# Kernel tuning notes

Hardware: AMD Instinct MI355X
Metric: run time of the kernel (lower is better)

Reference implementation:

```python
import jax, jax.numpy as jnp
import numpy as np

D_MODEL = 1024
NUM_HEADS = 16
D_K = D_MODEL // NUM_HEADS
D_FF = 4096
THETA = 10000.0
EPS = 1e-5


def rmsnorm(x, w):
    ms = jnp.mean(jnp.square(x), axis=-1, keepdims=True)
    return x * jax.lax.rsqrt(ms + EPS) * w


def rope(x, pos):
    # x: [B, H, S, d_k]; pos: [S]
    half = x.shape[-1] // 2
    inv_freq = THETA ** (-jnp.arange(half, dtype=x.dtype) * 2.0 / x.shape[-1])  # [half]
    ang = pos.astype(x.dtype)[:, None] * inv_freq[None, :]  # [S, half]
    cos, sin = jnp.cos(ang), jnp.sin(ang)
    xe, xo = x[..., 0::2], x[..., 1::2]
    oe = xe * cos - xo * sin
    oo = xe * sin + xo * cos
    return jnp.stack([oe, oo], axis=-1).reshape(x.shape)


def setup_inputs() -> dict:
    key = jax.random.key(0)
    ks = jax.random.split(key, 10)
    std_d = 1.0 / np.sqrt(D_MODEL)
    std_f = 1.0 / np.sqrt(D_FF)
    B, S = 4, 2048
    return {
        "x": jax.random.normal(ks[0], (B, S, D_MODEL), dtype=jnp.float32),
        "token_positions": jnp.arange(S, dtype=jnp.int32),
        "q_proj": jax.random.normal(ks[1], (D_MODEL, D_MODEL), dtype=jnp.float32) * std_d,
        "k_proj": jax.random.normal(ks[2], (D_MODEL, D_MODEL), dtype=jnp.float32) * std_d,
        "v_proj": jax.random.normal(ks[3], (D_MODEL, D_MODEL), dtype=jnp.float32) * std_d,
        "o_proj": jax.random.normal(ks[4], (D_MODEL, D_MODEL), dtype=jnp.float32) * std_d,
        "w1": jax.random.normal(ks[5], (D_FF, D_MODEL), dtype=jnp.float32) * std_d,
        "w2": jax.random.normal(ks[6], (D_MODEL, D_FF), dtype=jnp.float32) * std_f,
        "w3": jax.random.normal(ks[7], (D_FF, D_MODEL), dtype=jnp.float32) * std_d,
        "ln1_w": jnp.ones((D_MODEL,), dtype=jnp.float32),
        "ln2_w": jnp.ones((D_MODEL,), dtype=jnp.float32),
    }


def reference(x, token_positions, q_proj, k_proj, v_proj, o_proj, w1, w2, w3, ln1_w, ln2_w):
    B, S, _ = x.shape
    x_ln = rmsnorm(x, ln1_w)
    q = x_ln @ q_proj.T
    k = x_ln @ k_proj.T
    v = x_ln @ v_proj.T
    # [B, S, D] -> [B, H, S, d_k]
    def split_heads(t):
        return t.reshape(B, S, NUM_HEADS, D_K).transpose(0, 2, 1, 3)
    q, k, v = split_heads(q), split_heads(k), split_heads(v)
    q = rope(q, token_positions)
    k = rope(k, token_positions)
    scores = jnp.einsum("bhqd,bhkd->bhqk", q, k) / jnp.sqrt(jnp.asarray(D_K, x.dtype))
    causal = jnp.tril(jnp.ones((S, S), dtype=bool))
    scores = jnp.where(causal, scores, -jnp.inf)
    attn = jax.nn.softmax(scores, axis=-1)
    out = jnp.einsum("bhqk,bhkd->bhqd", attn, v)
    out = out.transpose(0, 2, 1, 3).reshape(B, S, D_MODEL)
    x = x + out @ o_proj.T
    x_ln2 = rmsnorm(x, ln2_w)
    u = x_ln2 @ w1.T
    vff = x_ln2 @ w3.T
    ff = (u * jax.nn.sigmoid(u)) * vff
    return x + ff @ w2.T
```

## Files before the change

kernel.cpp:

```cpp
#include <hip/hip_runtime.h>
#include <hip/hip_bf16.h>


typedef unsigned short u16;
typedef __attribute__((ext_vector_type(8))) short short8;
typedef __attribute__((ext_vector_type(4))) float f32x4;
typedef __attribute__((ext_vector_type(16))) float f32x16;

#define MFMA16(a, b, c) __builtin_amdgcn_mfma_f32_16x16x32_bf16(a, b, c, 0, 0, 0)
#define MFMA32(a, b, c) __builtin_amdgcn_mfma_f32_32x32x16_bf16(a, b, c, 0, 0, 0)

__device__ __forceinline__ u16 f2b(float f) {
  union { float f; unsigned u; } x; x.f = f;
  unsigned r = x.u + 0x7FFFu + ((x.u >> 16) & 1u);
  return (u16)(r >> 16);
}
__device__ __forceinline__ float b2f(u16 h) {
  union { unsigned u; float f; } x; x.u = ((unsigned)h) << 16;
  return x.f;
}
__device__ __forceinline__ unsigned pkbf(float a, float b) {
  __hip_bfloat162 h = __float22bfloat162_rn(make_float2(a, b));
  union { __hip_bfloat162 h; unsigned u; } cv; cv.h = h;
  return cv.u;
}
__device__ __forceinline__ void async16(const void* g, void* l) {
  __builtin_amdgcn_global_load_lds(
      (const __attribute__((address_space(1))) void*)g,
      (__attribute__((address_space(3))) void*)l, 16, 0, 0);
}

template <int MODE>
__global__ __launch_bounds__(256, 2) void gemm_bt(
    const u16* __restrict__ A, const u16* __restrict__ B,
    u16* __restrict__ Cb, float* __restrict__ Cf, const float* __restrict__ R,
    int M, int N, int K) {
  __shared__ __align__(16) u16 As[128 * 64];
  __shared__ __align__(16) u16 Bs[128 * 64];
  const int tid = threadIdx.x;
  const int l = tid & 63, w = tid >> 6;
  const int wr = w & 1, wc = w >> 1;
  const int lr = l & 31, lh = l >> 5;
  const size_t m0 = (size_t)blockIdx.y * 128, n0 = (size_t)blockIdx.x * 128;
  f32x16 acc[2][2] = {};
  for (int k0 = 0; k0 < K; k0 += 64) {
#pragma unroll
    for (int t = 0; t < 4; ++t) {
      int c = t * 256 + tid;
      int r = c >> 3;
      int gc = ((c & 7) ^ (r & 7)) << 3;
      async16(A + (m0 + r) * (size_t)K + k0 + gc, &As[c * 8]);
    }
#pragma unroll
    for (int t = 0; t < 4; ++t) {
      int c = t * 256 + tid;
      int r = c >> 3;
      int gc = ((c & 7) ^ (r & 7)) << 3;
      async16(B + (n0 + r) * (size_t)K + k0 + gc, &Bs[c * 8]);
    }
    __syncthreads();
#pragma unroll
    for (int c = 0; c < 4; ++c) {
      const int c8 = c * 2 + lh;
      short8 af[2], bfr[2];
#pragma unroll
      for (int mi = 0; mi < 2; ++mi) {
        int r = wr * 64 + mi * 32 + lr;
        af[mi] = *(const short8*)&As[r * 64 + ((c8 ^ (r & 7)) << 3)];
      }
#pragma unroll
      for (int ni = 0; ni < 2; ++ni) {
        int r = wc * 64 + ni * 32 + lr;
        bfr[ni] = *(const short8*)&Bs[r * 64 + ((c8 ^ (r & 7)) << 3)];
      }
#pragma unroll
      for (int mi = 0; mi < 2; ++mi)
#pragma unroll
        for (int ni = 0; ni < 2; ++ni)
          acc[mi][ni] = MFMA32(af[mi], bfr[ni], acc[mi][ni]);
    }
    __syncthreads();
  }
#pragma unroll
  for (int mi = 0; mi < 2; ++mi)
#pragma unroll
    for (int ni = 0; ni < 2; ++ni) {
      size_t n = n0 + wc * 64 + ni * 32 + lr;
#pragma unroll
      for (int reg = 0; reg < 16; ++reg) {
        size_t m = m0 + wr * 64 + mi * 32 + (reg & 3) + 8 * (reg >> 2) + 4 * lh;
        float v = acc[mi][ni][reg];
        if (MODE == 0)
          Cb[m * (size_t)N + n] = f2b(v);
        else
          Cf[m * (size_t)N + n] = v + R[m * (size_t)N + n];
      }
    }
}

__global__ __launch_bounds__(256, 2) void ffn_gemm(
    const u16* __restrict__ A, const u16* __restrict__ B1,
    const u16* __restrict__ B3, u16* __restrict__ Hout, int M, int N, int K) {
  __shared__ __align__(16) u16 As[128 * 64];
  __shared__ __align__(16) u16 B1s[128 * 64];
  __shared__ __align__(16) u16 B3s[128 * 64];
  const int tid = threadIdx.x;
  const int l = tid & 63, w = tid >> 6;
  const int wr = w & 1, wc = w >> 1;
  const int lr = l & 31, lh = l >> 5;
  const size_t m0 = (size_t)blockIdx.y * 128, n0 = (size_t)blockIdx.x * 128;
  f32x16 a1[2][2] = {}, a3[2][2] = {};
  for (int k0 = 0; k0 < K; k0 += 64) {
#pragma unroll
    for (int t = 0; t < 4; ++t) {
      int c = t * 256 + tid;
      int r = c >> 3;
      int gc = ((c & 7) ^ (r & 7)) << 3;
      async16(A + (m0 + r) * (size_t)K + k0 + gc, &As[c * 8]);
      async16(B1 + (n0 + r) * (size_t)K + k0 + gc, &B1s[c * 8]);
      async16(B3 + (n0 + r) * (size_t)K + k0 + gc, &B3s[c * 8]);
    }
    __syncthreads();
#pragma unroll
    for (int c = 0; c < 4; ++c) {
      const int c8 = c * 2 + lh;
      short8 af[2], b1f[2], b3f[2];
#pragma unroll
      for (int mi = 0; mi < 2; ++mi) {
        int r = wr * 64 + mi * 32 + lr;
        af[mi] = *(const short8*)&As[r * 64 + ((c8 ^ (r & 7)) << 3)];
      }
#pragma unroll
      for (int ni = 0; ni < 2; ++ni) {
        int r = wc * 64 + ni * 32 + lr;
        b1f[ni] = *(const short8*)&B1s[r * 64 + ((c8 ^ (r & 7)) << 3)];
        b3f[ni] = *(const short8*)&B3s[r * 64 + ((c8 ^ (r & 7)) << 3)];
      }
#pragma unroll
      for (int mi = 0; mi < 2; ++mi)
#pragma unroll
        for (int ni = 0; ni < 2; ++ni) {
          a1[mi][ni] = MFMA32(af[mi], b1f[ni], a1[mi][ni]);
          a3[mi][ni] = MFMA32(af[mi], b3f[ni], a3[mi][ni]);
        }
    }
    __syncthreads();
  }
#pragma unroll
  for (int mi = 0; mi < 2; ++mi)
#pragma unroll
    for (int ni = 0; ni < 2; ++ni) {
      size_t n = n0 + wc * 64 + ni * 32 + lr;
#pragma unroll
      for (int reg = 0; reg < 16; ++reg) {
        size_t m = m0 + wr * 64 + mi * 32 + (reg & 3) + 8 * (reg >> 2) + 4 * lh;
        float u = a1[mi][ni][reg];
        float g = u / (1.0f + __expf(-u));
        Hout[m * (size_t)N + n] = f2b(g * a3[mi][ni][reg]);
      }
    }
}

__global__ __launch_bounds__(256, 2) void attn_k(
    const u16* __restrict__ qh, const u16* __restrict__ kh,
    const u16* __restrict__ vt, u16* __restrict__ aout) {
  __shared__ __align__(16) u16 Ks[128 * 64];
  __shared__ __align__(16) u16 Vs[64 * 128];
  __shared__ __align__(16) u16 Ps[64 * 136];
  const int tid = threadIdx.x;
  const int l = tid & 63, w = tid >> 6;
  const int q = l & 15, lq = l >> 4;
  const int q0 = (int)(gridDim.x - 1 - blockIdx.x) * 128;
  const int bh = blockIdx.y;
  const size_t base = (size_t)bh * (2048 * 64);
  const int nt = (q0 >> 7) + 1;

  int qcol[2] = {q0 + w * 16 + q, q0 + 64 + w * 16 + q};
  short8 bq[2][2];
#pragma unroll
  for (int sub = 0; sub < 2; ++sub)
#pragma unroll
    for (int kk = 0; kk < 2; ++kk)
      bq[sub][kk] = *(const short8*)(qh + base + (size_t)qcol[sub] * 64 + kk * 32 + lq * 8);

  f32x4 o[2][4] = {};
  float mI[2] = {-1e30f, -1e30f}, lI[2] = {0.0f, 0.0f};
  u16* pr = &Ps[(w * 16 + q) * 136];

  for (int it = 0; it < nt; ++it) {
    const int kv0 = it << 7;
    if (it) __syncthreads();
#pragma unroll
    for (int t = 0; t < 4; ++t) {
      int p = t * 256 + tid;
      int r = p >> 3, cs = p & 7;
      async16(kh + base + (size_t)(kv0 + r) * 64 + ((cs ^ (r & 7)) << 3), &Ks[p * 8]);
    }
#pragma unroll
    for (int t = 0; t < 4; ++t) {
      int p = t * 256 + tid;
      int r = p >> 4, cs = p & 15;
      async16(vt + base + (size_t)r * 2048 + kv0 + ((cs ^ (r & 15)) << 3), &Vs[p * 8]);
    }
    __syncthreads();
    const bool last = (it == nt - 1);
#pragma unroll
    for (int sub = 0; sub < 2; ++sub) {
      f32x4 s[8] = {};
#pragma unroll
      for (int kk = 0; kk < 2; ++kk) {
#pragma unroll
        for (int mt = 0; mt < 8; ++mt) {
          int row = mt * 16 + q;
          short8 ak = *(const short8*)&Ks[row * 64 + (((kk * 4 + lq) ^ (q & 7)) << 3)];
          s[mt] = MFMA16(ak, bq[sub][kk], s[mt]);
        }
      }
      if (last) {
#pragma unroll
        for (int mt = 0; mt < 8; ++mt)
#pragma unroll
          for (int r = 0; r < 4; ++r)
            if (kv0 + mt * 16 + lq * 4 + r > qcol[sub]) s[mt][r] = -1e30f;
      }
      float mx = -1e30f;
#pragma unroll
      for (int mt = 0; mt < 8; ++mt)
#pragma unroll
        for (int r = 0; r < 4; ++r) mx = fmaxf(mx, s[mt][r]);
      mx = fmaxf(mx, __shfl_xor(mx, 16, 64));
      mx = fmaxf(mx, __shfl_xor(mx, 32, 64));
      const float mn = fmaxf(mI[sub], mx);
      const float al = exp2f(mI[sub] - mn);
      mI[sub] = mn;
      float rs = 0.0f;
#pragma unroll
      for (int mt = 0; mt < 8; ++mt)
#pragma unroll
        for (int r = 0; r < 4; ++r) {
          float p = exp2f(s[mt][r] - mn);
          s[mt][r] = p;
          rs += p;
        }
      rs += __shfl_xor(rs, 16, 64);
      rs += __shfl_xor(rs, 32, 64);
      lI[sub] = lI[sub] * al + rs;
#pragma unroll
      for (int mt = 0; mt < 4; ++mt)
#pragma unroll
        for (int r = 0; r < 4; ++r) o[sub][mt][r] *= al;
#pragma unroll
      for (int mt = 0; mt < 8; ++mt) {
        uint2 pd;
        pd.x = pkbf(s[mt][0], s[mt][1]);
        pd.y = pkbf(s[mt][2], s[mt][3]);
        *(uint2*)&pr[mt * 16 + lq * 4] = pd;
      }
#pragma unroll
      for (int kk = 0; kk < 4; ++kk) {
        short8 bp = *(const short8*)&pr[kk * 32 + lq * 8];
#pragma unroll
        for (int mt = 0; mt < 4; ++mt) {
          int row = mt * 16 + q;
          short8 av = *(const short8*)&Vs[row * 128 + (((kk * 4 + lq) ^ (row & 15)) << 3)];
          o[sub][mt] = MFMA16(av, bp, o[sub][mt]);
        }
      }
    }
  }
  const int b = bh >> 4, h = bh & 15;
#pragma unroll
  for (int sub = 0; sub < 2; ++sub) {
    const float inv = 1.0f / lI[sub];
#pragma unroll
    for (int mt = 0; mt < 4; ++mt) {
      uint2 pd;
      pd.x = pkbf(o[sub][mt][0] * inv, o[sub][mt][1] * inv);
      pd.y = pkbf(o[sub][mt][2] * inv, o[sub][mt][3] * inv);
      *(uint2*)&aout[((size_t)(b * 2048 + qcol[sub])) * 1024 + h * 64 + mt * 16 + lq * 4] = pd;
    }
  }
}

__global__ __launch_bounds__(256) void rmsnorm_k(
    const float* __restrict__ x, const float* __restrict__ w, u16* __restrict__ out) {
  const int row = blockIdx.x;
  const int tid = threadIdx.x;
  const float4 v = ((const float4*)(x + (size_t)row * 1024))[tid];
  float ss = v.x * v.x + v.y * v.y + v.z * v.z + v.w * v.w;
#pragma unroll
  for (int d = 1; d < 64; d <<= 1) ss += __shfl_xor(ss, d, 64);
  __shared__ float red[4];
  if ((tid & 63) == 0) red[tid >> 6] = ss;
  __syncthreads();
  const float sc = rsqrtf((red[0] + red[1] + red[2] + red[3]) * (1.0f / 1024.0f) + 1e-5f);
  const float4 wv = ((const float4*)w)[tid];
  u16* o = out + (size_t)row * 1024 + tid * 4;
  o[0] = f2b(v.x * sc * wv.x);
  o[1] = f2b(v.y * sc * wv.y);
  o[2] = f2b(v.z * sc * wv.z);
  o[3] = f2b(v.w * sc * wv.w);
}

__global__ __launch_bounds__(256) void rope_k(
    const u16* __restrict__ qkv, u16* __restrict__ qh, u16* __restrict__ kh,
    const int* __restrict__ pos) {
  int idx = blockIdx.x * 256 + threadIdx.x;
  int grp = idx & 255;
  int row = idx >> 8;
  int which = grp >> 7;
  int p = grp & 127;
  int s = row & 2047, b = row >> 11;
  int h = p >> 3, gi = p & 7;
  const u16* src = qkv + (size_t)row * 3072 + which * 1024 + h * 64 + gi * 8;
  uint4 in = *(const uint4*)src;
  const u16* e = (const u16*)&in;
  const float fp = (float)pos[s];
  const float scale = which ? 1.0f : 0.18033688011112042f;
  uint4 outv;
  unsigned* ov = (unsigned*)&outv;
#pragma unroll
  for (int j = 0; j < 4; ++j) {
    int i = gi * 4 + j;
    float xe = b2f(e[2 * j]), xo = b2f(e[2 * j + 1]);
    float inv = exp2f(-(float)(2 * i) * (13.287712379549449f / 64.0f));
    float ang = fp * inv;
    float sn, cs;
    __sincosf(ang, &sn, &cs);
    ov[j] = pkbf((xe * cs - xo * sn) * scale, (xe * sn + xo * cs) * scale);
  }
  u16* dst = (which ? kh : qh) + (((size_t)(b * 16 + h)) * 2048 + s) * 64 + gi * 8;
  *(uint4*)dst = outv;
}

__global__ __launch_bounds__(256) void transv_k(
    const u16* __restrict__ qkv, u16* __restrict__ vt) {
  __shared__ u16 t[64][65];
  const int bh = blockIdx.y, s0 = blockIdx.x * 64;
  const int b = bh >> 4, h = bh & 15;
  const int tid = threadIdx.x;
#pragma unroll
  for (int i = 0; i < 16; ++i) {
    int e = i * 256 + tid;
    int sl = e >> 6, d = e & 63;
    t[sl][d] = qkv[((size_t)(b * 2048 + s0 + sl)) * 3072 + 2048 + h * 64 + d];
  }
  __syncthreads();
#pragma unroll
  for (int i = 0; i < 16; ++i) {
    int e = i * 256 + tid;
    int d = e >> 6, sl = e & 63;
    vt[((size_t)(bh * 64 + d)) * 2048 + s0 + sl] = t[sl][d];
  }
}

__global__ __launch_bounds__(256) void cvt_all(
    const float* __restrict__ qp, const float* __restrict__ kp,
    const float* __restrict__ vp, const float* __restrict__ op,
    const float* __restrict__ w1, const float* __restrict__ w3,
    const float* __restrict__ w2,
    u16* __restrict__ WQKV, u16* __restrict__ WO,
    u16* __restrict__ W1, u16* __restrict__ W3, u16* __restrict__ W2) {
  int i = blockIdx.x * 256 + threadIdx.x;
  const float* src;
  u16* dst;
  int off;
  if (i < 1048576) {
    int seg = i >> 18, within = i & 262143;
    src = (seg == 0) ? qp : (seg == 1) ? kp : (seg == 2) ? vp : op;
    dst = (seg == 3) ? WO : WQKV + (size_t)seg * 1048576;
    off = within;
  } else {
    int j = i - 1048576;
    int seg = j >> 20;
    off = j & 1048575;
    src = (seg == 0) ? w1 : (seg == 1) ? w3 : w2;
    dst = (seg == 0) ? W1 : (seg == 1) ? W3 : W2;
  }
  float4 v = ((const float4*)src)[off];
  u16* o = dst + (size_t)off * 4;
  o[0] = f2b(v.x); o[1] = f2b(v.y); o[2] = f2b(v.z); o[3] = f2b(v.w);
}

extern "C" void kernel_launch(void* const* d_in, const int* in_sizes, int n_in,
                              void* d_out, int out_size, void* d_ws, size_t ws_size,
                              hipStream_t stream) {
  const float* x   = (const float*)d_in[0];
  const int*   pos = (const int*)d_in[1];
  const float* qp  = (const float*)d_in[2];
  const float* kp  = (const float*)d_in[3];
  const float* vp  = (const float*)d_in[4];
  const float* op  = (const float*)d_in[5];
  const float* w1  = (const float*)d_in[6];
  const float* w2  = (const float*)d_in[7];
  const float* w3  = (const float*)d_in[8];
  const float* ln1 = (const float*)d_in[9];
  const float* ln2 = (const float*)d_in[10];
  float* out = (float*)d_out;
  char* ws = (char*)d_ws;
  const size_t MB = 1024 * 1024;

  u16* WQKV = (u16*)(ws + 0 * MB);
  u16* WO   = (u16*)(ws + 6 * MB);
  u16* W1   = (u16*)(ws + 8 * MB);
  u16* W3   = (u16*)(ws + 16 * MB);
  u16* W2   = (u16*)(ws + 24 * MB);
  u16* XLN  = (u16*)(ws + 32 * MB);
  u16* QKV  = (u16*)(ws + 48 * MB);
  u16* QH   = (u16*)(ws + 96 * MB);
  u16* KH   = (u16*)(ws + 112 * MB);
  u16* VT   = (u16*)(ws + 128 * MB);
  u16* ATT  = (u16*)(ws + 48 * MB);
  u16* XLN2 = (u16*)(ws + 64 * MB);
  u16* Hbuf = (u16*)(ws + 80 * MB);
  (void)in_sizes; (void)n_in; (void)out_size; (void)ws_size;

  cvt_all<<<16384, 256, 0, stream>>>(qp, kp, vp, op, w1, w3, w2,
                                     WQKV, WO, W1, W3, W2);
  rmsnorm_k<<<8192, 256, 0, stream>>>(x, ln1, XLN);
  gemm_bt<0><<<dim3(24, 64), 256, 0, stream>>>(XLN, WQKV, QKV, nullptr, nullptr, 8192, 3072, 1024);
  rope_k<<<8192, 256, 0, stream>>>(QKV, QH, KH, pos);
  transv_k<<<dim3(32, 64), 256, 0, stream>>>(QKV, VT);
  attn_k<<<dim3(16, 64), 256, 0, stream>>>(QH, KH, VT, ATT);
  gemm_bt<1><<<dim3(8, 64), 256, 0, stream>>>(ATT, WO, nullptr, out, x, 8192, 1024, 1024);
  rmsnorm_k<<<8192, 256, 0, stream>>>(out, ln2, XLN2);
  ffn_gemm<<<dim3(32, 64), 256, 0, stream>>>(XLN2, W1, W3, Hbuf, 8192, 4096, 1024);
  gemm_bt<1><<<dim3(8, 64), 256, 0, stream>>>(Hbuf, W2, nullptr, out, out, 8192, 1024, 4096);
}
```

Measured before the change: 629.1 us.

## Double-buffer attention K/V tiles with smaller 64-wide blocks and new GEMM LDS swizzle

The attention kernel now uses 64-query blocks and 64-key tiles, with K/V tiles double-buffered in LDS. The next tile's async load is issued before the current tile is computed, so load latency overlaps with MFMA work, and the grid doubles so causal work is spread over more blocks. The GEMM and FFN LDS swizzle now XORs higher row bits into the column index, meant to cut bank conflicts on fragment reads. Smaller tiles mean more loop iterations and more sync overhead per unit of work. Nothing waits on the async loads explicitly beyond the barrier, so correctness depends on the barrier draining them.

```diff
diff --git a/kernel.cpp b/kernel.cpp
--- a/kernel.cpp
+++ b/kernel.cpp
@@ -9,6 +9,8 @@
 
 #define MFMA16(a, b, c) __builtin_amdgcn_mfma_f32_16x16x32_bf16(a, b, c, 0, 0, 0)
 #define MFMA32(a, b, c) __builtin_amdgcn_mfma_f32_32x32x16_bf16(a, b, c, 0, 0, 0)
+
+#define SWZ(r) (((r) ^ ((r) >> 3)) & 7)
 
 __device__ __forceinline__ u16 f2b(float f) {
   union { float f; unsigned u; } x; x.f = f;
@@ -48,14 +50,14 @@
     for (int t = 0; t < 4; ++t) {
       int c = t * 256 + tid;
       int r = c >> 3;
-      int gc = ((c & 7) ^ (r & 7)) << 3;
+      int gc = ((c & 7) ^ SWZ(r)) << 3;
       async16(A + (m0 + r) * (size_t)K + k0 + gc, &As[c * 8]);
     }
 #pragma unroll
     for (int t = 0; t < 4; ++t) {
       int c = t * 256 + tid;
       int r = c >> 3;
-      int gc = ((c & 7) ^ (r & 7)) << 3;
+      int gc = ((c & 7) ^ SWZ(r)) << 3;
       async16(B + (n0 + r) * (size_t)K + k0 + gc, &Bs[c * 8]);
     }
     __syncthreads();
@@ -66,12 +68,12 @@
 #pragma unroll
       for (int mi = 0; mi < 2; ++mi) {
         int r = wr * 64 + mi * 32 + lr;
-        af[mi] = *(const short8*)&As[r * 64 + ((c8 ^ (r & 7)) << 3)];
+        af[mi] = *(const short8*)&As[r * 64 + ((c8 ^ SWZ(r)) << 3)];
       }
 #pragma unroll
       for (int ni = 0; ni < 2; ++ni) {
         int r = wc * 64 + ni * 32 + lr;
-        bfr[ni] = *(const short8*)&Bs[r * 64 + ((c8 ^ (r & 7)) << 3)];
+        bfr[ni] = *(const short8*)&Bs[r * 64 + ((c8 ^ SWZ(r)) << 3)];
       }
 #pragma unroll
       for (int mi = 0; mi < 2; ++mi)
@@ -115,7 +117,7 @@
     for (int t = 0; t < 4; ++t) {
       int c = t * 256 + tid;
       int r = c >> 3;
-      int gc = ((c & 7) ^ (r & 7)) << 3;
+      int gc = ((c & 7) ^ SWZ(r)) << 3;
       async16(A + (m0 + r) * (size_t)K + k0 + gc, &As[c * 8]);
       async16(B1 + (n0 + r) * (size_t)K + k0 + gc, &B1s[c * 8]);
       async16(B3 + (n0 + r) * (size_t)K + k0 + gc, &B3s[c * 8]);
@@ -128,13 +130,13 @@
 #pragma unroll
       for (int mi = 0; mi < 2; ++mi) {
         int r = wr * 64 + mi * 32 + lr;
-        af[mi] = *(const short8*)&As[r * 64 + ((c8 ^ (r & 7)) << 3)];
+        af[mi] = *(const short8*)&As[r * 64 + ((c8 ^ SWZ(r)) << 3)];
       }
 #pragma unroll
       for (int ni = 0; ni < 2; ++ni) {
         int r = wc * 64 + ni * 32 + lr;
-        b1f[ni] = *(const short8*)&B1s[r * 64 + ((c8 ^ (r & 7)) << 3)];
-        b3f[ni] = *(const short8*)&B3s[r * 64 + ((c8 ^ (r & 7)) << 3)];
+        b1f[ni] = *(const short8*)&B1s[r * 64 + ((c8 ^ SWZ(r)) << 3)];
+        b3f[ni] = *(const short8*)&B3s[r * 64 + ((c8 ^ SWZ(r)) << 3)];
       }
 #pragma unroll
       for (int mi = 0; mi < 2; ++mi)
@@ -164,121 +166,122 @@
 __global__ __launch_bounds__(256, 2) void attn_k(
     const u16* __restrict__ qh, const u16* __restrict__ kh,
     const u16* __restrict__ vt, u16* __restrict__ aout) {
-  __shared__ __align__(16) u16 Ks[128 * 64];
-  __shared__ __align__(16) u16 Vs[64 * 128];
-  __shared__ __align__(16) u16 Ps[64 * 136];
+  __shared__ __align__(16) u16 Ks[2][64 * 64];
+  __shared__ __align__(16) u16 Vs[2][64 * 64];
+  __shared__ __align__(16) u16 Ps[64 * 72];
   const int tid = threadIdx.x;
   const int l = tid & 63, w = tid >> 6;
   const int q = l & 15, lq = l >> 4;
-  const int q0 = (int)(gridDim.x - 1 - blockIdx.x) * 128;
+  const int q0 = (int)(gridDim.x - 1 - blockIdx.x) * 64;
   const int bh = blockIdx.y;
   const size_t base = (size_t)bh * (2048 * 64);
-  const int nt = (q0 >> 7) + 1;
-
-  int qcol[2] = {q0 + w * 16 + q, q0 + 64 + w * 16 + q};
-  short8 bq[2][2];
-#pragma unroll
-  for (int sub = 0; sub < 2; ++sub)
-#pragma unroll
-    for (int kk = 0; kk < 2; ++kk)
-      bq[sub][kk] = *(const short8*)(qh + base + (size_t)qcol[sub] * 64 + kk * 32 + lq * 8);
-
-  f32x4 o[2][4] = {};
-  float mI[2] = {-1e30f, -1e30f}, lI[2] = {0.0f, 0.0f};
-  u16* pr = &Ps[(w * 16 + q) * 136];
-
-  for (int it = 0; it < nt; ++it) {
-    const int kv0 = it << 7;
-    if (it) __syncthreads();
-#pragma unroll
-    for (int t = 0; t < 4; ++t) {
+  const int nt = (q0 >> 6) + 1;
+  const int qcol = q0 + w * 16 + q;
+
+  short8 bq[2];
+#pragma unroll
+  for (int kk = 0; kk < 2; ++kk)
+    bq[kk] = *(const short8*)(qh + base + (size_t)qcol * 64 + kk * 32 + lq * 8);
+
+  f32x4 o[4] = {};
+  float mI = -1e30f, lI = 0.0f;
+  u16* pr = &Ps[(w * 16 + q) * 72];
+
+  {
+#pragma unroll
+    for (int t = 0; t < 2; ++t) {
       int p = t * 256 + tid;
       int r = p >> 3, cs = p & 7;
-      async16(kh + base + (size_t)(kv0 + r) * 64 + ((cs ^ (r & 7)) << 3), &Ks[p * 8]);
-    }
-#pragma unroll
-    for (int t = 0; t < 4; ++t) {
-      int p = t * 256 + tid;
-      int r = p >> 4, cs = p & 15;
-      async16(vt + base + (size_t)r * 2048 + kv0 + ((cs ^ (r & 15)) << 3), &Vs[p * 8]);
-    }
-    __syncthreads();
-    const bool last = (it == nt - 1);
-#pragma unroll
-    for (int sub = 0; sub < 2; ++sub) {
-      f32x4 s[8] = {};
-#pragma unroll
-      for (int kk = 0; kk < 2; ++kk) {
-#pragma unroll
-        for (int mt = 0; mt < 8; ++mt) {
-          int row = mt * 16 + q;
-          short8 ak = *(const short8*)&Ks[row * 64 + (((kk * 4 + lq) ^ (q & 7)) << 3)];
-          s[mt] = MFMA16(ak, bq[sub][kk], s[mt]);
-        }
-      }
-      if (last) {
-#pragma unroll
-        for (int mt = 0; mt < 8; ++mt)
-#pragma unroll
-          for (int r = 0; r < 4; ++r)
-            if (kv0 + mt * 16 + lq * 4 + r > qcol[sub]) s[mt][r] = -1e30f;
-      }
-      float mx = -1e30f;
-#pragma unroll
-      for (int mt = 0; mt < 8; ++mt)
-#pragma unroll
-        for (int r = 0; r < 4; ++r) mx = fmaxf(mx, s[mt][r]);
-      mx = fmaxf(mx, __shfl_xor(mx, 16, 64));
-      mx = fmaxf(mx, __shfl_xor(mx, 32, 64));
-      const float mn = fmaxf(mI[sub], mx);
-      const float al = exp2f(mI[sub] - mn);
-      mI[sub] = mn;
-      float rs = 0.0f;
-#pragma unroll
-      for (int mt = 0; mt < 8; ++mt)
-#pragma unroll
-        for (int r = 0; r < 4; ++r) {
-          float p = exp2f(s[mt][r] - mn);
-          s[mt][r] = p;
-          rs += p;
-        }
-      rs += __shfl_xor(rs, 16, 64);
-      rs += __shfl_xor(rs, 32, 64);
-      lI[sub] = lI[sub] * al + rs;
+      async16(kh + base + (size_t)r * 64 + ((cs ^ (r & 7)) << 3), &Ks[0][p * 8]);
+      async16(vt + base + (size_t)r * 2048 + ((cs ^ (r & 7)) << 3), &Vs[0][p * 8]);
+    }
+  }
+  __syncthreads();
+
+  for (int it = 0; it < nt; ++it) {
+    const int buf = it & 1;
+    if (it + 1 < nt) {
+      const int kn = (it + 1) << 6;
+#pragma unroll
+      for (int t = 0; t < 2; ++t) {
+        int p = t * 256 + tid;
+        int r = p >> 3, cs = p & 7;
+        async16(kh + base + (size_t)(kn + r) * 64 + ((cs ^ (r & 7)) << 3),
+                &Ks[buf ^ 1][p * 8]);
+        async16(vt + base + (size_t)r * 2048 + kn + ((cs ^ (r & 7)) << 3),
+                &Vs[buf ^ 1][p * 8]);
+      }
+    }
+    f32x4 s[4] = {};
+#pragma unroll
+    for (int kk = 0; kk < 2; ++kk) {
+#pragma unroll
+      for (int mt = 0; mt < 4; ++mt) {
+        int row = mt * 16 + q;
+        short8 ak = *(const short8*)&Ks[buf][row * 64 + (((kk * 4 + lq) ^ (row & 7)) << 3)];
+        s[mt] = MFMA16(ak, bq[kk], s[mt]);
+      }
+    }
+    if (it == nt - 1) {
+      const int kv0 = it << 6;
 #pragma unroll
       for (int mt = 0; mt < 4; ++mt)
 #pragma unroll
-        for (int r = 0; r < 4; ++r) o[sub][mt][r] *= al;
-#pragma unroll
-      for (int mt = 0; mt < 8; ++mt) {
-        uint2 pd;
-        pd.x = pkbf(s[mt][0], s[mt][1]);
-        pd.y = pkbf(s[mt][2], s[mt][3]);
-        *(uint2*)&pr[mt * 16 + lq * 4] = pd;
-      }
-#pragma unroll
-      for (int kk = 0; kk < 4; ++kk) {
-        short8 bp = *(const short8*)&pr[kk * 32 + lq * 8];
-#pragma unroll
-        for (int mt = 0; mt < 4; ++mt) {
-          int row = mt * 16 + q;
-          short8 av = *(const short8*)&Vs[row * 128 + (((kk * 4 + lq) ^ (row & 15)) << 3)];
-          o[sub][mt] = MFMA16(av, bp, o[sub][mt]);
-        }
-      }
-    }
-  }
-  const int b = bh >> 4, h = bh & 15;
-#pragma unroll
-  for (int sub = 0; sub < 2; ++sub) {
-    const float inv = 1.0f / lI[sub];
+        for (int r = 0; r < 4; ++r)
+          if (kv0 + mt * 16 + lq * 4 + r > qcol) s[mt][r] = -1e30f;
+    }
+    float mx = fmaxf(fmaxf(fmaxf(s[0][0], s[0][1]), fmaxf(s[0][2], s[0][3])),
+                     fmaxf(fmaxf(s[1][0], s[1][1]), fmaxf(s[1][2], s[1][3])));
+    mx = fmaxf(mx, fmaxf(fmaxf(fmaxf(s[2][0], s[2][1]), fmaxf(s[2][2], s[2][3])),
+                         fmaxf(fmaxf(s[3][0], s[3][1]), fmaxf(s[3][2], s[3][3]))));
+    mx = fmaxf(mx, __shfl_xor(mx, 16, 64));
+    mx = fmaxf(mx, __shfl_xor(mx, 32, 64));
+    const float mn = fmaxf(mI, mx);
+    const float al = exp2f(mI - mn);
+    mI = mn;
+    float rs = 0.0f;
+#pragma unroll
+    for (int mt = 0; mt < 4; ++mt)
+#pragma unroll
+      for (int r = 0; r < 4; ++r) {
+        float p = exp2f(s[mt][r] - mn);
+        s[mt][r] = p;
+        rs += p;
+      }
+    rs += __shfl_xor(rs, 16, 64);
+    rs += __shfl_xor(rs, 32, 64);
+    lI = lI * al + rs;
+#pragma unroll
+    for (int mt = 0; mt < 4; ++mt)
+#pragma unroll
+      for (int r = 0; r < 4; ++r) o[mt][r] *= al;
 #pragma unroll
     for (int mt = 0; mt < 4; ++mt) {
       uint2 pd;
-      pd.x = pkbf(o[sub][mt][0] * inv, o[sub][mt][1] * inv);
-      pd.y = pkbf(o[sub][mt][2] * inv, o[sub][mt][3] * inv);
-      *(uint2*)&aout[((size_t)(b * 2048 + qcol[sub])) * 1024 + h * 64 + mt * 16 + lq * 4] = pd;
-    }
+      pd.x = pkbf(s[mt][0], s[mt][1]);
+      pd.y = pkbf(s[mt][2], s[mt][3]);
+      *(uint2*)&pr[mt * 16 + lq * 4] = pd;
+    }
+#pragma unroll
+    for (int kk = 0; kk < 2; ++kk) {
+      short8 bp = *(const short8*)&pr[kk * 32 + lq * 8];
+#pragma unroll
+      for (int mt = 0; mt < 4; ++mt) {
+        int row = mt * 16 + q;
+        short8 av = *(const short8*)&Vs[buf][row * 64 + (((kk * 4 + lq) ^ (row & 7)) << 3)];
+        o[mt] = MFMA16(av, bp, o[mt]);
+      }
+    }
+    if (it + 1 < nt) __syncthreads();
+  }
+  const int b = bh >> 4, h = bh & 15;
+  const float inv = 1.0f / lI;
+#pragma unroll
+  for (int mt = 0; mt < 4; ++mt) {
+    uint2 pd;
+    pd.x = pkbf(o[mt][0] * inv, o[mt][1] * inv);
+    pd.y = pkbf(o[mt][2] * inv, o[mt][3] * inv);
+    *(uint2*)&aout[((size_t)(b * 2048 + qcol)) * 1024 + h * 64 + mt * 16 + lq * 4] = pd;
   }
 }
 
@@ -421,7 +424,7 @@
   gemm_bt<0><<<dim3(24, 64), 256, 0, stream>>>(XLN, WQKV, QKV, nullptr, nullptr, 8192, 3072, 1024);
   rope_k<<<8192, 256, 0, stream>>>(QKV, QH, KH, pos);
   transv_k<<<dim3(32, 64), 256, 0, stream>>>(QKV, VT);
-  attn_k<<<dim3(16, 64), 256, 0, stream>>>(QH, KH, VT, ATT);
+  attn_k<<<dim3(32, 64), 256, 0, stream>>>(QH, KH, VT, ATT);
   gemm_bt<1><<<dim3(8, 64), 256, 0, stream>>>(ATT, WO, nullptr, out, x, 8192, 1024, 1024);
   rmsnorm_k<<<8192, 256, 0, stream>>>(out, ln2, XLN2);
   ffn_gemm<<<dim3(32, 64), 256, 0, stream>>>(XLN2, W1, W3, Hbuf, 8192, 4096, 1024);
```

Measured after the change: 640.9 us. Within noise of the previous version (+1.9%).
